# Performance work log

Measured on AMD Instinct MI355X. Metric: run time of the kernel, lower is better.

The kernel has to match this reference:

```python
import jax, jax.numpy as jnp
import numpy as np

B = 128        # graphs
N_PER = 1024   # nodes per graph
K = 7          # knn neighbors
X_SIZE = 16
POS_SIZE = 3
H1, H2 = 64, 128
N = B * N_PER
EPS = 1e-5


def _lin_init(key, din, dout):
    kw, kb = jax.random.split(key)
    s = 1.0 / np.sqrt(din)
    w = jax.random.uniform(kw, (din, dout), jnp.float32, -s, s)
    b = jax.random.uniform(kb, (dout,), jnp.float32, -s, s)
    return w, b


def setup_inputs() -> dict:
    key = jax.random.key(0)
    ks = jax.random.split(key, 12)
    x = jax.random.normal(ks[0], (N, X_SIZE), jnp.float32)
    pos = jax.random.normal(ks[1], (N, POS_SIZE), jnp.float32)
    batch = jnp.repeat(jnp.arange(B, dtype=jnp.int32), N_PER)
    wk1, bk1 = _lin_init(ks[2], X_SIZE, H1)
    wq1, bq1 = _lin_init(ks[3], X_SIZE, H1)
    wv1, bv1 = _lin_init(ks[4], X_SIZE, H1)
    ws1, bs1 = _lin_init(ks[5], X_SIZE, H1)
    wk2, bk2 = _lin_init(ks[6], H1, H2)
    wq2, bq2 = _lin_init(ks[7], H1, H2)
    wv2, bv2 = _lin_init(ks[8], H1, H2)
    ws2, bs2 = _lin_init(ks[9], H1, H2)
    g1 = jnp.ones((H1,), jnp.float32); be1 = jnp.zeros((H1,), jnp.float32)
    g2 = jnp.ones((H2,), jnp.float32); be2 = jnp.zeros((H2,), jnp.float32)
    return dict(x=x, pos=pos, batch=batch,
                wk1=wk1, bk1=bk1, wq1=wq1, bq1=bq1, wv1=wv1, bv1=bv1, ws1=ws1, bs1=bs1, g1=g1, be1=be1,
                wk2=wk2, bk2=bk2, wq2=wq2, bq2=bq2, wv2=wv2, bv2=bv2, ws2=ws2, bs2=bs2, g2=g2, be2=be2)


def knn_edges(pos):
    # batch-aware kNN: graphs are equal-sized contiguous blocks of N_PER nodes
    p = pos.reshape(B, N_PER, POS_SIZE)
    def per_graph(pg):
        d = jnp.sum((pg[:, None, :] - pg[None, :, :]) ** 2, axis=-1)  # [n, n]
        d = jnp.where(jnp.eye(N_PER, dtype=bool), jnp.inf, d)          # no self loops
        _, idx = jax.lax.top_k(-d, K)                                   # [n, K]
        return idx
    idx = jax.vmap(per_graph)(p)                       # [B, N_PER, K]
    offs = (jnp.arange(B) * N_PER)[:, None, None]
    src = (idx + offs).reshape(-1)                     # neighbor j (source)
    dst = jnp.broadcast_to(jnp.arange(N_PER)[None, :, None] + offs, (B, N_PER, K)).reshape(-1)
    return src, dst


def res_gated_conv(x, src, dst, wk, bk, wq, bq, wv, bv, ws, bs):
    # out_i = skip(x_i) + sum_{j->i} sigmoid(K x_i + Q x_j) * V x_j
    kf = x @ wk + bk
    qf = x @ wq + bq
    vf = x @ wv + bv
    msg = jax.nn.sigmoid(kf[dst] + qf[src]) * vf[src]  # [E, out]
    agg = jnp.zeros_like(kf).at[dst].add(msg)
    return agg + x @ ws + bs


def batch_norm(x, gamma, beta):
    m = x.mean(0)
    v = jnp.mean((x - m) ** 2, 0)  # biased var (training-mode BN)
    return (x - m) * jax.lax.rsqrt(v + EPS) * gamma + beta


def reference(x, pos, batch, wk1, bk1, wq1, bq1, wv1, bv1, ws1, bs1, g1, be1,
              wk2, bk2, wq2, bq2, wv2, bv2, ws2, bs2, g2, be2):
    src, dst = knn_edges(pos)
    h = jax.nn.relu(batch_norm(res_gated_conv(x, src, dst, wk1, bk1, wq1, bq1, wv1, bv1, ws1, bs1), g1, be1))
    h = jax.nn.relu(batch_norm(res_gated_conv(h, src, dst, wk2, bk2, wq2, bq2, wv2, bv2, ws2, bs2), g2, be2))
    s = jax.ops.segment_sum(h, batch, num_segments=B)
    cnt = jax.ops.segment_sum(jnp.ones((h.shape[0], 1), h.dtype), batch, num_segments=B)
    return s / cnt
```

## Files before the change

kernel.cpp:

```cpp
#include <hip/hip_runtime.h>
#include <hip/hip_bf16.h>

#define BGR   128
#define NPER  1024
#define NK    7
#define NNODES (BGR*NPER)

typedef __attribute__((ext_vector_type(8))) short short8;
typedef __attribute__((ext_vector_type(8))) unsigned short ushort8;
typedef __attribute__((ext_vector_type(4))) float floatx4;

static __device__ __forceinline__ float bf2f(unsigned short u) {
    unsigned int x = ((unsigned int)u) << 16;
    return __builtin_bit_cast(float, x);
}
static __device__ __forceinline__ unsigned short f2bf(float f) {
    unsigned int x = __builtin_bit_cast(unsigned int, f);
    unsigned int lsb = (x >> 16) & 1u;
    x += 0x7fffu + lsb;
    return (unsigned short)(x >> 16);
}

__global__ __launch_bounds__(256) void knn_kernel(const float* __restrict__ pos,
                                                  int* __restrict__ idx) {
    __shared__ __align__(16) floatx4 sp[NPER];
    int g = blockIdx.x >> 2;
    int i_local = ((blockIdx.x & 3) << 8) + threadIdx.x;
    int base = g * NPER;
    const float* pg = pos + (size_t)base * 3;
    for (int t = threadIdx.x; t < NPER * 3; t += 256) {
        float v = pg[t];
        int j = t / 3, comp = t - j * 3;
        ((float*)&sp[j])[comp] = v;
    }
    __syncthreads();
    for (int j = threadIdx.x; j < NPER; j += 256) {
        floatx4 q = sp[j];
        sp[j].w = fmaf(q.x, q.x, fmaf(q.y, q.y, q.z * q.z));
    }
    __syncthreads();
    floatx4 me = sp[i_local];
    float m2x = -2.f * me.x, m2y = -2.f * me.y, m2z = -2.f * me.z;

    float b0=3e38f,b1=3e38f,b2=3e38f,b3=3e38f,b4=3e38f,b5=3e38f,b6=3e38f,b7=3e38f;
    for (int j0 = 0; j0 < NPER; j0 += 8) {
        #pragma unroll
        for (int u = 0; u < 8; ++u) {
            floatx4 q = sp[j0 + u];
            float d = fmaf(m2x, q.x, fmaf(m2y, q.y, fmaf(m2z, q.z, q.w)));
            unsigned int ub = (__builtin_bit_cast(unsigned int, d) & 0xFFFFFC00u)
                              | (unsigned int)(j0 + u);
            float t = __builtin_bit_cast(float, ub);
            float n7 = __builtin_amdgcn_fmed3f(b6, b7, t);
            float n6 = __builtin_amdgcn_fmed3f(b5, b6, t);
            float n5 = __builtin_amdgcn_fmed3f(b4, b5, t);
            float n4 = __builtin_amdgcn_fmed3f(b3, b4, t);
            float n3 = __builtin_amdgcn_fmed3f(b2, b3, t);
            float n2 = __builtin_amdgcn_fmed3f(b1, b2, t);
            float n1 = __builtin_amdgcn_fmed3f(b0, b1, t);
            b0 = fminf(b0, t);
            b1 = n1; b2 = n2; b3 = n3; b4 = n4; b5 = n5; b6 = n6; b7 = n7;
        }
    }
    int* op = idx + (size_t)(base + i_local) * NK;
    op[0] = base + (int)(__builtin_bit_cast(unsigned int, b1) & 1023u);
    op[1] = base + (int)(__builtin_bit_cast(unsigned int, b2) & 1023u);
    op[2] = base + (int)(__builtin_bit_cast(unsigned int, b3) & 1023u);
    op[3] = base + (int)(__builtin_bit_cast(unsigned int, b4) & 1023u);
    op[4] = base + (int)(__builtin_bit_cast(unsigned int, b5) & 1023u);
    op[5] = base + (int)(__builtin_bit_cast(unsigned int, b6) & 1023u);
    op[6] = base + (int)(__builtin_bit_cast(unsigned int, b7) & 1023u);
}

__global__ __launch_bounds__(256) void feat1_kernel(
    const float* __restrict__ x,
    const float* __restrict__ wk, const float* __restrict__ bk,
    const float* __restrict__ wq, const float* __restrict__ bq,
    const float* __restrict__ wv, const float* __restrict__ bv,
    const float* __restrict__ wsm, const float* __restrict__ bs,
    unsigned int* __restrict__ qv, unsigned int* __restrict__ ks) {
    int c = threadIdx.x & 63;
    float Wk[16], Wq[16], Wv[16], Ws[16];
    #pragma unroll
    for (int k = 0; k < 16; ++k) {
        Wk[k] = wk[k*64+c]; Wq[k] = wq[k*64+c]; Wv[k] = wv[k*64+c]; Ws[k] = wsm[k*64+c];
    }
    float Bk = bk[c], Bq = bq[c], Bv = bv[c], Bs = bs[c];
    int wave = blockIdx.x * (blockDim.x >> 6) + (threadIdx.x >> 6);
    int nw   = gridDim.x * (blockDim.x >> 6);
    for (int n = wave; n < NNODES; n += nw) {
        const float* xr = x + (size_t)n * 16;
        float ak = Bk, aq = Bq, av = Bv, as = Bs;
        #pragma unroll
        for (int k = 0; k < 16; ++k) {
            float xv = xr[k];
            ak += xv * Wk[k]; aq += xv * Wq[k]; av += xv * Wv[k]; as += xv * Ws[k];
        }
        size_t o = (size_t)n * 64 + c;
        qv[o] = ((unsigned int)f2bf(av) << 16) | f2bf(aq);
        ks[o] = ((unsigned int)f2bf(as) << 16) | f2bf(ak);
    }
}

template<int C>
__global__ __launch_bounds__(256) void conv_kernel(
    const unsigned int* __restrict__ qv, const unsigned int* __restrict__ ks,
    const int* __restrict__ idx, unsigned short* __restrict__ h,
    float* __restrict__ part) {
    const int NPB = 256 / C;
    int c   = threadIdx.x & (C - 1);
    int sub = __builtin_amdgcn_readfirstlane((int)(threadIdx.x / C));
    int b     = blockIdx.x;
    int xcd   = b & 7;
    int chunk = b >> 3;
    int graph = xcd * 16 + (chunk >> 5);
    int nblk  = chunk & 31;
    int n0 = graph * NPER + nblk * 32;
    float s = 0.f, s2 = 0.f;
    #pragma unroll 2
    for (int i = sub; i < 32; i += NPB) {
        int n = n0 + i;
        const int* nb = idx + (size_t)n * NK;
        unsigned int ku = ks[(size_t)n * C + c];
        float kv  = bf2f((unsigned short)(ku & 0xFFFF));
        float acc = bf2f((unsigned short)(ku >> 16));
        #pragma unroll
        for (int k = 0; k < NK; ++k) {
            int j = __builtin_amdgcn_readfirstlane(nb[k]);
            const unsigned int* p = qv + (size_t)j * C;
            unsigned int u = p[c];
            float qvv = bf2f((unsigned short)(u & 0xFFFF));
            float vvv = bf2f((unsigned short)(u >> 16));
            float t = kv + qvv;
            float sg = __builtin_amdgcn_rcpf(1.f + __expf(-t));
            acc = fmaf(sg, vvv, acc);
        }
        unsigned short hb = f2bf(acc);
        h[(size_t)n * C + c] = hb;
        float hv = bf2f(hb);
        s += hv; s2 += hv * hv;
    }
    __shared__ float ls[256], ls2[256];
    ls[threadIdx.x] = s; ls2[threadIdx.x] = s2;
    __syncthreads();
    if (threadIdx.x < C) {
        #pragma unroll
        for (int l = 1; l < NPB; ++l) { s += ls[threadIdx.x + l*C]; s2 += ls2[threadIdx.x + l*C]; }
        part[(size_t)blockIdx.x * 2 * C + threadIdx.x]     = s;
        part[(size_t)blockIdx.x * 2 * C + C + threadIdx.x] = s2;
    }
}

template<int C>
static __device__ __forceinline__ void bnfin_body(
    const float* __restrict__ part, const float* __restrict__ gamma,
    const float* __restrict__ beta, float* __restrict__ ss,
    int c, float* ls, float* ls2) {
    float s = 0.f, s2 = 0.f;
    for (int b = threadIdx.x; b < 4096; b += 256) {
        s  += part[(size_t)b * 2 * C + c];
        s2 += part[(size_t)b * 2 * C + C + c];
    }
    ls[threadIdx.x] = s; ls2[threadIdx.x] = s2;
    __syncthreads();
    for (int st = 128; st > 0; st >>= 1) {
        if (threadIdx.x < st) { ls[threadIdx.x] += ls[threadIdx.x+st]; ls2[threadIdx.x] += ls2[threadIdx.x+st]; }
        __syncthreads();
    }
    if (threadIdx.x == 0) {
        float m   = ls[0] / (float)NNODES;
        float var = ls2[0] / (float)NNODES - m * m;
        float inv = rsqrtf(var + 1e-5f);
        float sc  = gamma[c] * inv;
        ss[c]     = sc;
        ss[C + c] = beta[c] - m * sc;
    }
}

template<int C>
__global__ __launch_bounds__(256) void bnfin_kernel(
    const float* __restrict__ part, const float* __restrict__ gamma,
    const float* __restrict__ beta, float* __restrict__ ss) {
    __shared__ float ls[256], ls2[256];
    bnfin_body<C>(part, gamma, beta, ss, blockIdx.x, ls, ls2);
}

__global__ __launch_bounds__(256) void fin1_wfrag_kernel(
    const float* __restrict__ part, const float* __restrict__ gamma,
    const float* __restrict__ beta, float* __restrict__ ss,
    const float* __restrict__ w0, const float* __restrict__ w1,
    const float* __restrict__ w2, const float* __restrict__ w3,
    unsigned short* __restrict__ frag) {
    __shared__ float ls[256], ls2[256];
    if (blockIdx.x < 64) {
        bnfin_body<64>(part, gamma, beta, ss, blockIdx.x, ls, ls2);
        return;
    }
    int s  = blockIdx.x - 64;
    if (threadIdx.x >= 64) return;
    int m  = s >> 4;
    int kt = (s >> 3) & 1;
    int ct = s & 7;
    const float* w = (m == 0) ? w0 : (m == 1) ? w1 : (m == 2) ? w2 : w3;
    int l = threadIdx.x;
    int col = ct * 16 + (l & 15);
    int kbase = kt * 32 + (l >> 4) * 8;
    unsigned short* out = frag + ((size_t)s * 64 + l) * 8;
    #pragma unroll
    for (int e = 0; e < 8; ++e) out[e] = f2bf(w[(size_t)(kbase + e) * 128 + col]);
}

__global__ __launch_bounds__(256) void feat2_kernel(
    const unsigned short* __restrict__ h1n, const unsigned short* __restrict__ frag,
    const float* __restrict__ ss1,
    const float* __restrict__ b0, const float* __restrict__ b1,
    const float* __restrict__ b2, const float* __restrict__ b3,
    unsigned int* __restrict__ qv2, unsigned int* __restrict__ ks2) {
    __shared__ unsigned short xh[2][2][16][17];
    int nt = blockIdx.x;
    int m  = threadIdx.x >> 6;
    int l  = threadIdx.x & 63;
    const float* bm = (m == 0) ? b0 : (m == 1) ? b1 : (m == 2) ? b2 : b3;
    int lr = l & 15;
    int gq = l >> 4;
    int n  = nt * 16 + lr;
    const unsigned short* ar = h1n + (size_t)n * 64 + gq * 8;
    short8 a0r = *(const short8*)ar;
    short8 a1r = *(const short8*)(ar + 32);
    short8 a0, a1;
    #pragma unroll
    for (int e = 0; e < 8; ++e) {
        int c0 = gq * 8 + e;
        float f0 = bf2f((unsigned short)a0r[e]) * ss1[c0] + ss1[64 + c0];
        a0[e] = (short)f2bf(fmaxf(f0, 0.f));
        int c1 = 32 + gq * 8 + e;
        float f1 = bf2f((unsigned short)a1r[e]) * ss1[c1] + ss1[64 + c1];
        a1[e] = (short)f2bf(fmaxf(f1, 0.f));
    }
    #pragma unroll
    for (int ct = 0; ct < 8; ++ct) {
        size_t fb0 = ((size_t)(m * 16 + ct)     * 64 + l) * 8;
        size_t fb1 = ((size_t)(m * 16 + 8 + ct) * 64 + l) * 8;
        short8 w0 = *(const short8*)(frag + fb0);
        short8 w1 = *(const short8*)(frag + fb1);
        float bv = bm[ct * 16 + lr];
        floatx4 acc = {bv, bv, bv, bv};
        acc = __builtin_amdgcn_mfma_f32_16x16x32_bf16(a0, w0, acc, 0, 0, 0);
        acc = __builtin_amdgcn_mfma_f32_16x16x32_bf16(a1, w1, acc, 0, 0, 0);
        if (m >= 2) {
            #pragma unroll
            for (int r = 0; r < 4; ++r)
                xh[ct & 1][m - 2][gq * 4 + r][lr] = f2bf(acc[r]);
        }
        __syncthreads();
        if (m < 2) {
            unsigned int* od = (m == 1) ? qv2 : ks2;
            int set = (m == 1) ? 0 : 1;
            #pragma unroll
            for (int r = 0; r < 4; ++r) {
                unsigned int lo = f2bf(acc[r]);
                unsigned int hi = xh[ct & 1][set][gq * 4 + r][lr];
                od[(size_t)(nt * 16 + gq * 4 + r) * 128 + ct * 16 + lr] = (hi << 16) | lo;
            }
        }
    }
}

__global__ __launch_bounds__(256) void pool_partial_kernel(const unsigned short* __restrict__ h2,
                                                           const float* __restrict__ ss2,
                                                           float* __restrict__ part) {
    int g = blockIdx.x >> 2;
    int q = blockIdx.x & 3;
    int c = threadIdx.x & 127;
    int isub = threadIdx.x >> 7;
    float sc = ss2[c], sh = ss2[128 + c];
    float acc = 0.f;
    const unsigned short* hp = h2 + ((size_t)g * NPER + q * 256) * 128;
    for (int i = isub; i < 256; i += 2)
        acc += fmaxf(bf2f(hp[(size_t)i * 128 + c]) * sc + sh, 0.f);
    __shared__ float red[256];
    red[threadIdx.x] = acc;
    __syncthreads();
    if (threadIdx.x < 128)
        part[(size_t)blockIdx.x * 128 + c] = acc + red[threadIdx.x + 128];
}

__global__ void pool_final_kernel(const float* __restrict__ part, float* __restrict__ out) {
    int g = blockIdx.x, c = threadIdx.x;
    float s = part[(size_t)(g*4+0)*128+c] + part[(size_t)(g*4+1)*128+c]
            + part[(size_t)(g*4+2)*128+c] + part[(size_t)(g*4+3)*128+c];
    out[(size_t)g * 128 + c] = s * (1.f / 1024.f);
}

extern "C" void kernel_launch(void* const* d_in, const int* in_sizes, int n_in,
                              void* d_out, int out_size, void* d_ws, size_t ws_size,
                              hipStream_t stream) {
    const float* x   = (const float*)d_in[0];
    const float* pos = (const float*)d_in[1];
    const float* wk1 = (const float*)d_in[3];
    const float* bk1 = (const float*)d_in[4];
    const float* wq1 = (const float*)d_in[5];
    const float* bq1 = (const float*)d_in[6];
    const float* wv1 = (const float*)d_in[7];
    const float* bv1 = (const float*)d_in[8];
    const float* ws1 = (const float*)d_in[9];
    const float* bs1 = (const float*)d_in[10];
    const float* g1  = (const float*)d_in[11];
    const float* be1 = (const float*)d_in[12];
    const float* wk2 = (const float*)d_in[13];
    const float* bk2 = (const float*)d_in[14];
    const float* wq2 = (const float*)d_in[15];
    const float* bq2 = (const float*)d_in[16];
    const float* wv2 = (const float*)d_in[17];
    const float* bv2 = (const float*)d_in[18];
    const float* ws2 = (const float*)d_in[19];
    const float* bs2 = (const float*)d_in[20];
    const float* g2  = (const float*)d_in[21];
    const float* be2 = (const float*)d_in[22];
    float* out = (float*)d_out;

    const size_t SZ_QV1 = (size_t)NNODES * 64 * 4;
    const size_t SZ_QV2 = (size_t)NNODES * 128 * 4;

    char* ws = (char*)d_ws;
    size_t off = 0;
    auto alloc = [&](size_t b) { size_t o = off; off += (b + 255) & ~(size_t)255; return o; };

    int* idx              = (int*)(ws + alloc((size_t)NNODES * NK * 4));
    size_t o_region       = alloc(2 * SZ_QV2);
    unsigned int* qv1     = (unsigned int*)(ws + o_region);
    unsigned int* ks1     = (unsigned int*)(ws + o_region + SZ_QV1);
    unsigned int* qv2     = (unsigned int*)(ws + o_region);
    unsigned int* ks2     = (unsigned int*)(ws + o_region + SZ_QV2);
    unsigned short* h1    = (unsigned short*)(ws + alloc((size_t)NNODES * 64 * 2));
    unsigned short* h2    = (unsigned short*)(ws + alloc((size_t)NNODES * 128 * 2));
    unsigned short* frag  = (unsigned short*)(ws + alloc(64 * 64 * 8 * 2));
    float* part           = (float*)(ws + alloc((size_t)4096 * 2 * 128 * 4));
    float* ss1            = (float*)(ws + alloc(2 * 64 * 4));
    float* ss2            = (float*)(ws + alloc(2 * 128 * 4));
    (void)ws_size; (void)in_sizes; (void)n_in; (void)out_size;

    knn_kernel<<<BGR * 4, 256, 0, stream>>>(pos, idx);
    feat1_kernel<<<1024, 256, 0, stream>>>(x, wk1, bk1, wq1, bq1, wv1, bv1, ws1, bs1,
                                           qv1, ks1);
    conv_kernel<64><<<NNODES / 32, 256, 0, stream>>>(qv1, ks1, idx, h1, part);
    fin1_wfrag_kernel<<<128, 256, 0, stream>>>(part, g1, be1, ss1,
                                               wk2, wq2, wv2, ws2, frag);
    feat2_kernel<<<NNODES / 16, 256, 0, stream>>>(h1, frag, ss1, bk2, bq2, bv2, bs2,
                                                  qv2, ks2);
    conv_kernel<128><<<NNODES / 32, 256, 0, stream>>>(qv2, ks2, idx, h2, part);
    bnfin_kernel<128><<<128, 256, 0, stream>>>(part, g2, be2, ss2);
    pool_partial_kernel<<<BGR * 4, 256, 0, stream>>>(h2, ss2, part);
    pool_final_kernel<<<BGR, 128, 0, stream>>>(part, out);
}
```

Measured before the change: 259.7 us.

## Split kNN candidate scan across two half-blocks and merge partial top-k

Each block now handles 128 query points instead of 256. The two halves of the block each scan half of the 1024 candidates, which halves the serial insertion loop per thread and doubles the grid to 1024 blocks. The partial sorted top-8 lists go through shared memory and are combined with a bitonic-style min merge. The half that contains the query drops its self entry. The aim is higher occupancy and shorter per-thread latency in the kNN stage, at the cost of loading the positions twice as often, an extra barrier and an unsorted neighbour order.

```diff
diff --git a/kernel.cpp b/kernel.cpp
--- a/kernel.cpp
+++ b/kernel.cpp
@@ -24,9 +24,10 @@
 __global__ __launch_bounds__(256) void knn_kernel(const float* __restrict__ pos,
                                                   int* __restrict__ idx) {
     __shared__ __align__(16) floatx4 sp[NPER];
-    int g = blockIdx.x >> 2;
-    int i_local = ((blockIdx.x & 3) << 8) + threadIdx.x;
-    int base = g * NPER;
+    __shared__ float ex[256][9];
+    int g     = blockIdx.x >> 3;
+    int qbase = (blockIdx.x & 7) << 7;
+    int base  = g * NPER;
     const float* pg = pos + (size_t)base * 3;
     for (int t = threadIdx.x; t < NPER * 3; t += 256) {
         float v = pg[t];
@@ -39,11 +40,15 @@
         sp[j].w = fmaf(q.x, q.x, fmaf(q.y, q.y, q.z * q.z));
     }
     __syncthreads();
-    floatx4 me = sp[i_local];
+
+    int qi = qbase + (threadIdx.x & 127);
+    int hf = threadIdx.x >> 7;
+    floatx4 me = sp[qi];
     float m2x = -2.f * me.x, m2y = -2.f * me.y, m2z = -2.f * me.z;
 
     float b0=3e38f,b1=3e38f,b2=3e38f,b3=3e38f,b4=3e38f,b5=3e38f,b6=3e38f,b7=3e38f;
-    for (int j0 = 0; j0 < NPER; j0 += 8) {
+    int j0base = hf << 9;
+    for (int j0 = j0base; j0 < j0base + 512; j0 += 8) {
         #pragma unroll
         for (int u = 0; u < 8; ++u) {
             floatx4 q = sp[j0 + u];
@@ -62,14 +67,20 @@
             b1 = n1; b2 = n2; b3 = n3; b4 = n4; b5 = n5; b6 = n6; b7 = n7;
         }
     }
-    int* op = idx + (size_t)(base + i_local) * NK;
-    op[0] = base + (int)(__builtin_bit_cast(unsigned int, b1) & 1023u);
-    op[1] = base + (int)(__builtin_bit_cast(unsigned int, b2) & 1023u);
-    op[2] = base + (int)(__builtin_bit_cast(unsigned int, b3) & 1023u);
-    op[3] = base + (int)(__builtin_bit_cast(unsigned int, b4) & 1023u);
-    op[4] = base + (int)(__builtin_bit_cast(unsigned int, b5) & 1023u);
-    op[5] = base + (int)(__builtin_bit_cast(unsigned int, b6) & 1023u);
-    op[6] = base + (int)(__builtin_bit_cast(unsigned int, b7) & 1023u);
+    float* er = ex[threadIdx.x];
+    er[0]=b0; er[1]=b1; er[2]=b2; er[3]=b3; er[4]=b4; er[5]=b5; er[6]=b6; er[7]=b7;
+    __syncthreads();
+    if (threadIdx.x < 128) {
+        int sh = qi >> 9;
+        const float* A  = ex[threadIdx.x + (sh << 7)];
+        const float* Bo = ex[threadIdx.x + ((1 - sh) << 7)];
+        int* op = idx + (size_t)(base + qi) * NK;
+        #pragma unroll
+        for (int i = 0; i < 7; ++i) {
+            float mm = fminf(A[i + 1], Bo[6 - i]);
+            op[i] = base + (int)(__builtin_bit_cast(unsigned int, mm) & 1023u);
+        }
+    }
 }
 
 __global__ __launch_bounds__(256) void feat1_kernel(
@@ -340,7 +351,7 @@
     float* ss2            = (float*)(ws + alloc(2 * 128 * 4));
     (void)ws_size; (void)in_sizes; (void)n_in; (void)out_size;
 
-    knn_kernel<<<BGR * 4, 256, 0, stream>>>(pos, idx);
+    knn_kernel<<<BGR * 8, 256, 0, stream>>>(pos, idx);
     feat1_kernel<<<1024, 256, 0, stream>>>(x, wk1, bk1, wq1, bq1, wv1, bv1, ws1, bs1,
                                            qv1, ks1);
     conv_kernel<64><<<NNODES / 32, 256, 0, stream>>>(qv1, ks1, idx, h1, part);
```

Result: no change. 257.3 us (-0.9%).
